# Performance work log

Measured on AMD Instinct MI355X. Metric: run time of the kernel, lower is better.

## Reference

```python
import jax, jax.numpy as jnp
import numpy as np

B, T, NMELS = 2, 2048, 64
D, H, DH, M, L = 256, 4, 64, 384, 4
FF2 = 2 * 4 * D  # GLU doubles the 4*dim hidden


def _layernorm(x, g, b):
    m = x.mean(-1, keepdims=True)
    v = ((x - m) ** 2).mean(-1, keepdims=True)
    return (x - m) * jax.lax.rsqrt(v + 1e-5) * g + b


def _conv(h, w, groups=1, pad='VALID'):
    return jax.lax.conv_general_dilated(h, w, (1, 1), pad, feature_group_count=groups,
                                        dimension_numbers=('NCHW', 'OIHW', 'NCHW'))


def _bn(h, g, b, m, v):
    return (h - m[:, None, None]) * jax.lax.rsqrt(v[:, None, None] + 1e-5) * g[:, None, None] + b[:, None, None]


def setup_inputs():
    key = jax.random.key(0)
    ks = jax.random.split(key, 40)
    def n(i, shape, s):
        return (jax.random.normal(ks[i], shape) * s).astype(jnp.float32)
    z = lambda shape: jnp.zeros(shape, jnp.float32)
    o = lambda shape: jnp.ones(shape, jnp.float32)
    return dict(
        x=n(0, (B, T, NMELS), 1.0),
        conv0_w=n(1, (4, 1, 1, 1), 0.5),
        dw1_w=n(2, (4, 1, 3, 3), 0.3), dw1_b=z(4),
        pw1_w=n(3, (D // 2, 4, 1, 1), 0.5), pw1_b=z(D // 2),
        bn1_g=o(D // 2), bn1_b=z(D // 2), bn1_m=n(4, (D // 2,), 0.05), bn1_v=o(D // 2),
        dw2_w=n(5, (D // 2, 1, 3, 3), 0.3), dw2_b=z(D // 2),
        pw2_w=n(6, (D, D // 2, 1, 1), 0.1), pw2_b=z(D),
        bn2_g=o(D), bn2_b=z(D), bn2_m=n(7, (D,), 0.05), bn2_v=o(D),
        proj_w=n(8, (D, D), 0.06), proj_b=z(D),
        ln0_g=o(D), ln0_b=z(D),
        pos_emb=n(9, (1, T, D), 0.02),
        ln1_g=o((L, D)), ln1_b=z((L, D)),
        wq=n(10, (L, D, D), 0.06), bq=z((L, D)),
        wk=n(11, (L, D, D), 0.06), bk=z((L, D)),
        wv=n(12, (L, D, D), 0.06), bv=z((L, D)),
        wo=n(13, (L, D, D), 0.06), bo=z((L, D)),
        proj_mat=n(14, (L, M, DH), 1.0),
        ln2_g=o((L, D)), ln2_b=z((L, D)),
        ffw1=n(15, (L, D, FF2), 0.06), ffb1=z((L, FF2)),
        ffw2=n(16, (L, FF2 // 2, D), 0.03), ffb2=z((L, D)),
        clf_w1=n(17, (D, D // 2), 0.06), clf_b1=z(D // 2),
        clf_ln_g=o(D // 2), clf_ln_b=z(D // 2),
        clf_w2=n(18, (D // 2, 1), 0.09), clf_b2=z(1),
    )


def reference(x, conv0_w, dw1_w, dw1_b, pw1_w, pw1_b, bn1_g, bn1_b, bn1_m, bn1_v,
              dw2_w, dw2_b, pw2_w, pw2_b, bn2_g, bn2_b, bn2_m, bn2_v,
              proj_w, proj_b, ln0_g, ln0_b, pos_emb,
              ln1_g, ln1_b, wq, bq, wk, bk, wv, bv, wo, bo, proj_mat,
              ln2_g, ln2_b, ffw1, ffb1, ffw2, ffb2,
              clf_w1, clf_b1, clf_ln_g, clf_ln_b, clf_w2, clf_b2):
    pad1 = ((1, 1), (1, 1))
    # conv frontend: [B,T,n_mels] -> [B,1,n_mels,T]
    h = x.transpose(0, 2, 1)[:, None]
    h = _conv(h, conv0_w)
    h = _conv(h, dw1_w, groups=4, pad=pad1) + dw1_b[:, None, None]
    h = _conv(h, pw1_w) + pw1_b[:, None, None]
    h = jax.nn.relu(_bn(h, bn1_g, bn1_b, bn1_m, bn1_v))
    h = _conv(h, dw2_w, groups=D // 2, pad=pad1) + dw2_b[:, None, None]
    h = _conv(h, pw2_w) + pw2_b[:, None, None]
    h = jax.nn.relu(_bn(h, bn2_g, bn2_b, bn2_m, bn2_v))
    h = h.mean(axis=2).transpose(0, 2, 1)  # [B,T,D]
    h = h @ proj_w + proj_b
    h = _layernorm(h, ln0_g, ln0_b) + pos_emb[:, :h.shape[1]]
    # reversible Performer: streams x1 (attn) / x2 (ff), combined by sum
    x1, x2 = h, h
    dn = DH ** -0.25
    for l in range(L):
        a = _layernorm(x2, ln1_g[l], ln1_b[l])
        Bsz, N, _ = a.shape
        q = (a @ wq[l] + bq[l]).reshape(Bsz, N, H, DH).transpose(0, 2, 1, 3)
        k = (a @ wk[l] + bk[l]).reshape(Bsz, N, H, DH).transpose(0, 2, 1, 3)
        v = (a @ wv[l] + bv[l]).reshape(Bsz, N, H, DH).transpose(0, 2, 1, 3)
        # FAVOR+ generalized (ReLU) kernel feature maps, eps=1e-3
        qf = jax.nn.relu(jnp.einsum('bhnd,jd->bhnj', dn * q, proj_mat[l])) + 1e-3
        kf = jax.nn.relu(jnp.einsum('bhnd,jd->bhnj', dn * k, proj_mat[l])) + 1e-3
        d_inv = 1.0 / jnp.einsum('bhnj,bhj->bhn', qf, kf.sum(axis=2))
        ctx = jnp.einsum('bhnj,bhnd->bhjd', kf, v)
        o = jnp.einsum('bhjd,bhnj,bhn->bhnd', ctx, qf, d_inv)
        o = o.transpose(0, 2, 1, 3).reshape(Bsz, N, D)
        x1 = x1 + (o @ wo[l] + bo[l])
        f = _layernorm(x1, ln2_g[l], ln2_b[l])
        u1, u2 = jnp.split(f @ ffw1[l] + ffb1[l], 2, axis=-1)
        x2 = x2 + (jax.nn.gelu(u1, approximate=False) * u2) @ ffw2[l] + ffb2[l]
    h = x1 + x2
    c = jax.nn.relu(_layernorm(h @ clf_w1 + clf_b1, clf_ln_g, clf_ln_b))
    return (c @ clf_w2 + clf_b2)[..., 0]
```

## Files before the change

kernel.cpp:

```cpp
#include <hip/hip_runtime.h>
#include <hip/hip_bf16.h>
#include <math.h>

using bf16 = __hip_bfloat16;
typedef __attribute__((ext_vector_type(8))) short short8;
typedef __attribute__((ext_vector_type(4))) float f32x4;

__device__ __forceinline__ float tof(float x) { return x; }
__device__ __forceinline__ float tof(bf16 x) { return __bfloat162float(x); }
__device__ __forceinline__ float b2f(unsigned short u) {
  union { float f; unsigned int i; } c; c.i = ((unsigned int)u) << 16; return c.f;
}
__device__ __forceinline__ unsigned short f2bu(float v) {
  bf16 h = __float2bfloat16(v);
  return *(unsigned short*)&h;
}
__device__ __forceinline__ void sto1(float* p, float v) { *p = v; }
__device__ __forceinline__ void sto1(bf16* p, float v) { *p = __float2bfloat16(v); }

__device__ __forceinline__ float gelu_exact(float x) {
  return 0.5f * x * (1.f + erff(x * 0.70710678118654752f));
}

__device__ __forceinline__ void llds16(const bf16* g, short* l) {
  __builtin_amdgcn_global_load_lds((const __attribute__((address_space(1))) void*)g,
                                   (__attribute__((address_space(3))) void*)l, 16, 0, 0);
}


__global__ __launch_bounds__(256) void pack_qkv3_kernel(
    const float* __restrict__ wq, const float* __restrict__ wk,
    const float* __restrict__ wv, bf16* __restrict__ out)
{
  int idx = blockIdx.x * 256 + threadIdx.x;
  int k = idx & 255;
  int nl = idx >> 8;
  int n = nl % 768, l = nl / 768;
  const float* src = (n < 256) ? wq : (n < 512 ? wk : wv);
  float v = src[(long)l * 65536 + k * 256 + (n & 255)];
  unsigned short hi = f2bu(v);
  unsigned short lo = f2bu(v - b2f(hi));
  unsigned short* o = (unsigned short*)out + (long)l * 589824 + (long)n * 768;
  o[k] = hi; o[256 + k] = hi; o[512 + k] = lo;
}

__global__ __launch_bounds__(256) void pack_qkvbias_kernel(
    const float* __restrict__ bq, const float* __restrict__ bk,
    const float* __restrict__ bv, float* __restrict__ out)
{
  int i = blockIdx.x * 256 + threadIdx.x;
  if (i >= 3072) return;
  int n = i % 768, l = i / 768;
  const float* src = (n < 256) ? bq : (n < 512 ? bk : bv);
  out[i] = src[l * 256 + (n & 255)];
}

__global__ __launch_bounds__(256) void tconv_kernel(
    const float* __restrict__ in, bf16* __restrict__ out,
    int K, int N, long sin, long sout)
{
  int l = blockIdx.z;
  int idx = blockIdx.x * 256 + threadIdx.x;
  int k = idx % K, n = idx / K;
  out[l * sout + idx] = __float2bfloat16(in[l * sin + (long)k * N + n]);
}

__global__ __launch_bounds__(256) void tconv3_kernel(
    const float* __restrict__ in, bf16* __restrict__ out,
    int K, int N, long sin, long sout)
{
  int l = blockIdx.z;
  int idx = blockIdx.x * 256 + threadIdx.x;
  int k = idx % K, n = idx / K;
  float v = in[l * sin + (long)k * N + n];
  unsigned short hi = f2bu(v);
  unsigned short lo = f2bu(v - b2f(hi));
  unsigned short* o = (unsigned short*)out + l * sout + (long)n * (3 * K);
  o[k] = hi; o[K + k] = hi; o[2 * K + k] = lo;
}

__global__ __launch_bounds__(256) void f2b_kernel(
    const float* __restrict__ in, bf16* __restrict__ out, int n)
{
  int i = blockIdx.x * 256 + threadIdx.x;
  if (i < n) out[i] = __float2bfloat16(in[i]);
}

__global__ __launch_bounds__(256) void zero4_kernel(float* __restrict__ p) {
  int i = (blockIdx.x * 256 + threadIdx.x) * 4;
  float4 z; z.x = 0.f; z.y = 0.f; z.z = 0.f; z.w = 0.f;
  *(float4*)&p[i] = z;
}

__global__ __launch_bounds__(256) void sumb3_kernel(
    const float* __restrict__ a, const float* __restrict__ b, bf16* __restrict__ o)
{
  int row = blockIdx.x, c = threadIdx.x;
  long i = (long)row * 256 + c;
  float v = a[i] + b[i];
  unsigned short hi = f2bu(v);
  unsigned short lo = f2bu(v - b2f(hi));
  unsigned short* op = (unsigned short*)o + (long)row * 768 + c;
  op[0] = hi; op[256] = lo; op[512] = hi;
}

__global__ __launch_bounds__(256) void front1_kernel(
    const float* __restrict__ x, const float* __restrict__ c0w,
    const float* __restrict__ d1w, const float* __restrict__ d1b,
    const float* __restrict__ p1w, const float* __restrict__ p1b,
    const float* __restrict__ g1, const float* __restrict__ b1,
    const float* __restrict__ m1, const float* __restrict__ v1,
    bf16* __restrict__ A1)
{
  __shared__ float sd[256];
  __shared__ float ss[128], st[128], sb[128];
  int tid = threadIdx.x;
  int bt = ((blockIdx.x & 7) << 9) | (blockIdx.x >> 3);
  int b = bt >> 11, t = bt & 2047;
  if (tid < 128) {
    float s = g1[tid] * rsqrtf(v1[tid] + 1e-5f);
    ss[tid] = s;
    st[tid] = b1[tid] - m1[tid] * s;
    sb[tid] = p1b[tid];
  }
  {
    int c = tid >> 6, f = tid & 63;
    float cw = c0w[c];
    float acc = d1b[c];
#pragma unroll
    for (int kh = 0; kh < 3; ++kh) {
      int fi = f + kh - 1;
      if (fi < 0 || fi >= 64) continue;
#pragma unroll
      for (int kw = 0; kw < 3; ++kw) {
        int ti = t + kw - 1;
        if (ti < 0 || ti >= 2048) continue;
        acc += d1w[c * 9 + kh * 3 + kw] * cw * x[((long)b * 2048 + ti) * 64 + fi];
      }
    }
    sd[c * 64 + f] = acc;
  }
  int ci0 = (tid * 8) & 127;
  float wreg[8][4];
#pragma unroll
  for (int j = 0; j < 8; ++j) {
    f32x4 w4 = *(const f32x4*)&p1w[(ci0 + j) * 4];
#pragma unroll
    for (int c = 0; c < 4; ++c) wreg[j][c] = w4[c];
  }
  __syncthreads();
  float ssr[8], str[8], sbr[8];
#pragma unroll
  for (int j = 0; j < 8; ++j) {
    ssr[j] = ss[ci0 + j]; str[j] = st[ci0 + j]; sbr[j] = sb[ci0 + j];
  }
  long ob = (long)bt * 8192;
  unsigned short* A1u = (unsigned short*)A1;
#pragma unroll
  for (int it = 0; it < 4; ++it) {
    int f = it * 16 + (tid >> 4);
    float sdv[4];
#pragma unroll
    for (int c = 0; c < 4; ++c) sdv[c] = sd[c * 64 + f];
    short8 pkt;
#pragma unroll
    for (int j = 0; j < 8; ++j) {
      float pre = sbr[j];
#pragma unroll
      for (int c = 0; c < 4; ++c) pre = fmaf(wreg[j][c], sdv[c], pre);
      pkt[j] = (short)f2bu(fmaxf(fmaf(ssr[j], pre, str[j]), 0.f));
    }
    *(short8*)&A1u[ob + it * 2048 + tid * 8] = pkt;
  }
}

__global__ __launch_bounds__(256, 4) void convtail_kernel(
    const bf16* __restrict__ A1, const float* __restrict__ w,
    const float* __restrict__ wb, const bf16* __restrict__ w2b,
    const float* __restrict__ pb, const float* __restrict__ g2,
    const float* __restrict__ b2, const float* __restrict__ m2,
    const float* __restrict__ v2, bf16* __restrict__ hconv3)
{
  __shared__ short dw2s[64 * 136];
  __shared__ short Bs[64 * 136];
  __shared__ float red[1024];
  __shared__ float ssc[64], ssh[64];
  int tid = threadIdx.x;
  int lane = tid & 63, wv = tid >> 6;
  int quad = lane >> 4, l15 = lane & 15;
  int rw = (wv >> 1) * 32, cw = (wv & 1) * 32;
  int bt = ((blockIdx.x & 7) << 9) | (blockIdx.x >> 3);
  int b = bt >> 11, t = bt & 2047;
  int ci8 = (tid & 15) * 8;
  float wreg[9][8], breg[8];
#pragma unroll
  for (int c = 0; c < 8; ++c) {
    breg[c] = wb[ci8 + c];
#pragma unroll
    for (int kk = 0; kk < 9; ++kk) wreg[kk][c] = w[(ci8 + c) * 9 + kk];
  }
  const unsigned short* A1u = (const unsigned short*)A1;
  for (int pass = 0; pass < 4; ++pass) {
    int f = pass * 16 + (tid >> 4);
    float a[8];
#pragma unroll
    for (int c = 0; c < 8; ++c) a[c] = breg[c];
#pragma unroll
    for (int kh = 0; kh < 3; ++kh) {
      int fi = f + kh - 1;
      if (fi < 0 || fi >= 64) continue;
#pragma unroll
      for (int kw = 0; kw < 3; ++kw) {
        int ti = t + kw - 1;
        if (ti < 0 || ti >= 2048) continue;
        short8 u = *(const short8*)&A1u[(((long)b * 2048 + ti) * 64 + fi) * 128 + ci8];
        int kk = kh * 3 + kw;
#pragma unroll
        for (int c = 0; c < 8; ++c)
          a[c] = fmaf(wreg[kk][c], b2f((unsigned short)u[c]), a[c]);
      }
    }
    short8 p;
#pragma unroll
    for (int c = 0; c < 8; ++c) p[c] = (short)f2bu(a[c]);
    *(short8*)&dw2s[f * 136 + ci8] = p;
  }
  for (int ct = 0; ct < 4; ++ct) {
    int co0 = ct * 64;
    __syncthreads();
    for (int l2 = 0; l2 < 4; ++l2) {
      int idx = l2 * 256 + tid;
      int row = idx >> 4, koff = (idx & 15) * 8;
      *(short8*)&Bs[row * 136 + koff] =
          *(const short8*)&w2b[(long)(co0 + row) * 128 + koff];
    }
    if (tid < 64) {
      int co = co0 + tid;
      float s = g2[co] * rsqrtf(v2[co] + 1e-5f);
      ssc[tid] = s;
      ssh[tid] = b2[co] - m2[co] * s + s * pb[co];
    }
    __syncthreads();
    f32x4 zv = {0.f, 0.f, 0.f, 0.f};
    f32x4 acc[2][2] = {{zv, zv}, {zv, zv}};
#pragma unroll
    for (int kc = 0; kc < 4; ++kc) {
      short8 a0 = *(const short8*)&dw2s[(rw + l15) * 136 + kc * 32 + quad * 8];
      short8 a1 = *(const short8*)&dw2s[(rw + 16 + l15) * 136 + kc * 32 + quad * 8];
      short8 b0 = *(const short8*)&Bs[(cw + l15) * 136 + kc * 32 + quad * 8];
      short8 b1 = *(const short8*)&Bs[(cw + 16 + l15) * 136 + kc * 32 + quad * 8];
      acc[0][0] = __builtin_amdgcn_mfma_f32_16x16x32_bf16(a0, b0, acc[0][0], 0, 0, 0);
      acc[0][1] = __builtin_amdgcn_mfma_f32_16x16x32_bf16(a0, b1, acc[0][1], 0, 0, 0);
      acc[1][0] = __builtin_amdgcn_mfma_f32_16x16x32_bf16(a1, b0, acc[1][0], 0, 0, 0);
      acc[1][1] = __builtin_amdgcn_mfma_f32_16x16x32_bf16(a1, b1, acc[1][1], 0, 0, 0);
    }
#pragma unroll
    for (int mi = 0; mi < 2; ++mi)
#pragma unroll
      for (int nj = 0; nj < 2; ++nj) {
        int colg = cw + nj * 16 + l15;
        float s = ssc[colg], sh = ssh[colg];
        float sum = 0.f;
#pragma unroll
        for (int r = 0; r < 4; ++r) sum += fmaxf(fmaf(s, acc[mi][nj][r], sh), 0.f);
        int rowgroup = (wv >> 1) * 8 + mi * 4 + quad;
        red[rowgroup * 64 + colg] = sum;
      }
    __syncthreads();
    if (tid < 64) {
      float s = 0.f;
#pragma unroll
      for (int r = 0; r < 16; ++r) s += red[r * 64 + tid];
      float vo = s * (1.f / 64.f);
      unsigned short hi = f2bu(vo);
      unsigned short lo = f2bu(vo - b2f(hi));
      unsigned short* hp = (unsigned short*)hconv3 + (long)bt * 768 + co0 + tid;
      hp[0] = hi; hp[256] = lo; hp[512] = hi;
    }
  }
}

__global__ __launch_bounds__(256) void favor_kernel(
    const bf16* __restrict__ qkvb, const bf16* __restrict__ pm,
    bf16* __restrict__ qf, bf16* __restrict__ kfT, float dn)
{
  __shared__ short As[4096];
  __shared__ short Bs[4096];
  int tid = threadIdx.x;
  int lane = tid & 63, w = tid >> 6;
  int quad = lane >> 4, l15 = lane & 15;
  int rw = (w >> 1) * 32, cw = (w & 1) * 32;
  int r0 = blockIdx.x * 64, n0 = blockIdx.y * 64;
  int z16 = blockIdx.z;
  bool isK = z16 >= 8;
  int z = z16 & 7, zb = z >> 2, zh = z & 3;
  const bf16* A = qkvb + (isK ? 256 : 0) + (long)zb * 1048576 + zh * 64;
  f32x4 zv = {0.f, 0.f, 0.f, 0.f};
  f32x4 acc[2][2] = {{zv, zv}, {zv, zv}};
  const bf16* Ag = A + (long)(r0 + (tid >> 2)) * 512 + ((tid & 3) * 8);
  const bf16* Bg = pm + (long)(n0 + (tid >> 2)) * 64 + ((tid & 3) * 8);
  llds16(Ag, &As[tid * 8]);
  llds16(Ag + 32, &As[tid * 8 + 2048]);
  llds16(Bg, &Bs[tid * 8]);
  llds16(Bg + 32, &Bs[tid * 8 + 2048]);
  __syncthreads();
#pragma unroll
  for (int c = 0; c < 2; ++c) {
    short8 a0 = *(const short8*)&As[c * 2048 + (rw + l15) * 32 + quad * 8];
    short8 a1 = *(const short8*)&As[c * 2048 + (rw + 16 + l15) * 32 + quad * 8];
    short8 b0 = *(const short8*)&Bs[c * 2048 + (cw + l15) * 32 + quad * 8];
    short8 b1 = *(const short8*)&Bs[c * 2048 + (cw + 16 + l15) * 32 + quad * 8];
    acc[0][0] = __builtin_amdgcn_mfma_f32_16x16x32_bf16(a0, b0, acc[0][0], 0, 0, 0);
    acc[0][1] = __builtin_amdgcn_mfma_f32_16x16x32_bf16(a0, b1, acc[0][1], 0, 0, 0);
    acc[1][0] = __builtin_amdgcn_mfma_f32_16x16x32_bf16(a1, b0, acc[1][0], 0, 0, 0);
    acc[1][1] = __builtin_amdgcn_mfma_f32_16x16x32_bf16(a1, b1, acc[1][1], 0, 0, 0);
  }
  bf16* qfz = qf + (long)zb * 3145728 + (long)zh * 786432;
  unsigned short* kfz = (unsigned short*)kfT + (long)zb * 3145728 + (long)zh * 786432;
#pragma unroll
  for (int mi = 0; mi < 2; ++mi)
#pragma unroll
    for (int nj = 0; nj < 2; ++nj) {
      int colg = n0 + cw + nj * 16 + l15;
      int rbase = r0 + rw + mi * 16 + quad * 4;
      float ov[4];
#pragma unroll
      for (int r = 0; r < 4; ++r)
        ov[r] = fmaxf(acc[mi][nj][r] * dn, 0.f) + 1e-3f;
      if (!isK) {
#pragma unroll
        for (int r = 0; r < 4; ++r)
          qfz[(long)(rbase + r) * 384 + colg] = __float2bfloat16(ov[r]);
      } else {
        ushort4 p;
        p.x = f2bu(ov[0]); p.y = f2bu(ov[1]); p.z = f2bu(ov[2]); p.w = f2bu(ov[3]);
        *(ushort4*)&kfz[(long)colg * 2048 + rbase] = p;
      }
    }
}

__global__ __launch_bounds__(256) void rowsum_kernel(
    const bf16* __restrict__ kfT, float* __restrict__ ksum)
{
  int z = blockIdx.x;
  int j = blockIdx.y * 4 + (threadIdx.x >> 6);
  int lane = threadIdx.x & 63;
  const short* base = (const short*)kfT + ((long)z * 384 + j) * 2048;
  float acc = 0.f;
#pragma unroll
  for (int i = 0; i < 4; ++i) {
    short8 v = *(const short8*)&base[i * 512 + lane * 8];
#pragma unroll
    for (int e = 0; e < 8; ++e) acc += b2f((unsigned short)v[e]);
  }
#pragma unroll
  for (int o = 32; o > 0; o >>= 1) acc += __shfl_xor(acc, o, 64);
  if (lane == 0) ksum[z * 384 + j] = acc;
}

template <typename CTy, int EPI>
__global__ __launch_bounds__(256) void mgemm_kernel(
    const bf16* __restrict__ A, const bf16* __restrict__ Bt,
    const float* __restrict__ bias, const float* __restrict__ res,
    const float* __restrict__ rowsc, CTy* __restrict__ C, bf16* __restrict__ C2,
    int K, int lda, int ldbt, int ldc,
    long sAb, long sAh, long sBb, long sBh, long sCb, long sCh,
    long sRb, long sRh, int Hdiv, float alpha)
{
  __shared__ short As[4096];
  __shared__ short Bs[4096];
  __shared__ short Bs2[(EPI == 8) ? 4096 : 8];
  int tid = threadIdx.x;
  int lane = tid & 63, w = tid >> 6;
  int quad = lane >> 4, l15 = lane & 15;
  int rw = (w >> 1) * 32, cw = (w & 1) * 32;
  int r0 = blockIdx.x * 64, n0 = blockIdx.y * 64;
  int zb = blockIdx.z / Hdiv, zh = blockIdx.z % Hdiv;
  A += zb * sAb + zh * sAh;
  Bt += zb * sBb + zh * sBh;
  C += zb * sCb + zh * sCh;
  if (res) res += zb * sCb + zh * sCh;
  const float* rsp = (EPI == 3) ? rowsc + zb * sRb + zh * sRh : nullptr;
  f32x4 zv = {0.f, 0.f, 0.f, 0.f};
  f32x4 acc[2][2] = {{zv, zv}, {zv, zv}};
  f32x4 acc2[2][2] = {{zv, zv}, {zv, zv}};
  const bf16* Ag = A + (long)(r0 + (tid >> 2)) * lda + ((tid & 3) * 8);
  const bf16* Bg = Bt + (long)(n0 + (tid >> 2)) * ldbt + ((tid & 3) * 8);
  const bf16* Bg2 = (EPI == 8) ? Bg + sRb : nullptr;
  short* Asd = &As[tid * 8];
  short* Bsd = &Bs[tid * 8];
  short* Bs2d = &Bs2[(EPI == 8) ? tid * 8 : 0];
  for (int k0 = 0; k0 < K; k0 += 64) {
    if (k0) __syncthreads();
    llds16(Ag + k0, Asd);
    llds16(Ag + k0 + 32, Asd + 2048);
    llds16(Bg + k0, Bsd);
    llds16(Bg + k0 + 32, Bsd + 2048);
    if constexpr (EPI == 8) {
      llds16(Bg2 + k0, Bs2d);
      llds16(Bg2 + k0 + 32, Bs2d + 2048);
    }
    __syncthreads();
#pragma unroll
    for (int c = 0; c < 2; ++c) {
      short8 a0 = *(const short8*)&As[c * 2048 + (rw + l15) * 32 + quad * 8];
      short8 a1 = *(const short8*)&As[c * 2048 + (rw + 16 + l15) * 32 + quad * 8];
      short8 b0 = *(const short8*)&Bs[c * 2048 + (cw + l15) * 32 + quad * 8];
      short8 b1 = *(const short8*)&Bs[c * 2048 + (cw + 16 + l15) * 32 + quad * 8];
      acc[0][0] = __builtin_amdgcn_mfma_f32_16x16x32_bf16(a0, b0, acc[0][0], 0, 0, 0);
      acc[0][1] = __builtin_amdgcn_mfma_f32_16x16x32_bf16(a0, b1, acc[0][1], 0, 0, 0);
      acc[1][0] = __builtin_amdgcn_mfma_f32_16x16x32_bf16(a1, b0, acc[1][0], 0, 0, 0);
      acc[1][1] = __builtin_amdgcn_mfma_f32_16x16x32_bf16(a1, b1, acc[1][1], 0, 0, 0);
      if constexpr (EPI == 8) {
        short8 c0 = *(const short8*)&Bs2[c * 2048 + (cw + l15) * 32 + quad * 8];
        short8 c1 = *(const short8*)&Bs2[c * 2048 + (cw + 16 + l15) * 32 + quad * 8];
        acc2[0][0] = __builtin_amdgcn_mfma_f32_16x16x32_bf16(a0, c0, acc2[0][0], 0, 0, 0);
        acc2[0][1] = __builtin_amdgcn_mfma_f32_16x16x32_bf16(a0, c1, acc2[0][1], 0, 0, 0);
        acc2[1][0] = __builtin_amdgcn_mfma_f32_16x16x32_bf16(a1, c0, acc2[1][0], 0, 0, 0);
        acc2[1][1] = __builtin_amdgcn_mfma_f32_16x16x32_bf16(a1, c1, acc2[1][1], 0, 0, 0);
      }
    }
  }
#pragma unroll
  for (int mi = 0; mi < 2; ++mi)
#pragma unroll
    for (int nj = 0; nj < 2; ++nj) {
      int colg = n0 + cw + nj * 16 + l15;
      float bv_ = bias ? bias[colg] : 0.f;
      float bv2 = (EPI == 8) ? bias[colg + 1024] : 0.f;
      int rbase = r0 + rw + mi * 16 + quad * 4;
      float ov[4];
#pragma unroll
      for (int r = 0; r < 4; ++r) {
        float v = acc[mi][nj][r];
        if constexpr (EPI == 0 || EPI == 5) {
          v += bv_;
        } else if constexpr (EPI == 1) {
          v += bv_ + res[(long)(rbase + r) * ldc + colg];
        } else if constexpr (EPI == 3) {
          v *= rsp[rbase + r];
        } else if constexpr (EPI == 7) {
          if (zh == 0) v += bv_;
        } else if constexpr (EPI == 8) {
          v = gelu_exact(v + bv_) * (acc2[mi][nj][r] + bv2);
        }
        ov[r] = v;
      }
      if constexpr (EPI == 5) {
        if (colg < 512) {
#pragma unroll
          for (int r = 0; r < 4; ++r) sto1(&C[(long)(rbase + r) * ldc + colg], ov[r]);
        } else {
          int bb = rbase >> 11, t0 = rbase & 2047;
          long off = (((long)bb * 4 + ((colg - 512) >> 6)) * 64 + (colg & 63)) * 2048 + t0;
          ushort4 p;
          p.x = f2bu(ov[0]); p.y = f2bu(ov[1]); p.z = f2bu(ov[2]); p.w = f2bu(ov[3]);
          *(ushort4*)((unsigned short*)C2 + off) = p;
        }
      } else if constexpr (EPI == 7) {
#pragma unroll
        for (int r = 0; r < 4; ++r)
          atomicAdd((float*)&C[(long)(rbase + r) * ldc + colg], ov[r]);
      } else if constexpr (EPI == 8) {
        unsigned short* Cu = (unsigned short*)C;
#pragma unroll
        for (int r = 0; r < 4; ++r) {
          float v = ov[r];
          unsigned short hi = f2bu(v);
          unsigned short lo = f2bu(v - b2f(hi));
          long rowo = (long)(rbase + r) * ldc;
          Cu[rowo + colg] = hi;
          Cu[rowo + 1024 + colg] = lo;
          Cu[rowo + 2048 + colg] = hi;
        }
      } else {
#pragma unroll
        for (int r = 0; r < 4; ++r) sto1(&C[(long)(rbase + r) * ldc + colg], ov[r]);
      }
    }
  (void)alpha;
}

template <int DIM, bool RELU, bool ADDPOS, bool DUAL, bool A3, typename OTy>
__global__ __launch_bounds__(256) void ln_kernel(
    const float* __restrict__ in, const float* __restrict__ g,
    const float* __restrict__ b, const float* __restrict__ pos,
    OTy* __restrict__ out0, float* __restrict__ out1)
{
  constexpr int CH = DIM / 64;
  int row = blockIdx.x * 4 + (threadIdx.x >> 6);
  int lane = threadIdx.x & 63;
  const float* rp = in + (long)row * DIM + lane * CH;
  float v[CH];
#pragma unroll
  for (int i = 0; i < CH; ++i) v[i] = rp[i];
  float s = 0.f;
#pragma unroll
  for (int i = 0; i < CH; ++i) s += v[i];
#pragma unroll
  for (int o = 32; o > 0; o >>= 1) s += __shfl_xor(s, o, 64);
  float mean = s * (1.f / DIM);
  float q = 0.f;
#pragma unroll
  for (int i = 0; i < CH; ++i) { float d = v[i] - mean; q += d * d; }
#pragma unroll
  for (int o = 32; o > 0; o >>= 1) q += __shfl_xor(q, o, 64);
  float rstd = rsqrtf(q * (1.f / DIM) + 1e-5f);
  int t = row & 2047;
#pragma unroll
  for (int i = 0; i < CH; ++i) {
    int c = lane * CH + i;
    float o = (v[i] - mean) * rstd * g[c] + b[c];
    if constexpr (ADDPOS) o += pos[(long)t * DIM + c];
    if constexpr (RELU) o = fmaxf(o, 0.f);
    if constexpr (A3) {
      unsigned short hi = f2bu(o);
      unsigned short lo = f2bu(o - b2f(hi));
      unsigned short* op = (unsigned short*)out0 + (long)row * (3 * DIM) + c;
      op[0] = hi; op[DIM] = lo; op[2 * DIM] = hi;
    } else {
      sto1(&out0[(long)row * DIM + c], o);
      if constexpr (DUAL) out1[(long)row * DIM + c] = o;
    }
  }
}

__global__ __launch_bounds__(256) void dinv_kernel(
    const bf16* __restrict__ qf, const float* __restrict__ ksum,
    float* __restrict__ dinv)
{
  int z = blockIdx.x;
  int t = blockIdx.y * 4 + (threadIdx.x >> 6);
  int lane = threadIdx.x & 63;
  const bf16* qr = qf + ((long)z * 2048 + t) * 384;
  const float* ks = ksum + z * 384;
  float acc = 0.f;
#pragma unroll
  for (int i = 0; i < 6; ++i) {
    int j = lane + i * 64;
    acc = fmaf(tof(qr[j]), ks[j], acc);
  }
#pragma unroll
  for (int o = 32; o > 0; o >>= 1) acc += __shfl_xor(acc, o, 64);
  if (lane == 0) dinv[z * 2048 + t] = 1.f / acc;
}

__global__ __launch_bounds__(256) void clf2_kernel(
    const float* __restrict__ c2, const float* __restrict__ w,
    const float* __restrict__ b, float* __restrict__ out)
{
  int row = blockIdx.x * 4 + (threadIdx.x >> 6);
  int lane = threadIdx.x & 63;
  const float* rp = c2 + (long)row * 128 + lane * 2;
  float acc = rp[0] * w[lane * 2] + rp[1] * w[lane * 2 + 1];
#pragma unroll
  for (int o = 32; o > 0; o >>= 1) acc += __shfl_xor(acc, o, 64);
  if (lane == 0) out[row] = acc + b[0];
}

extern "C" void kernel_launch(void* const* d_in, const int* in_sizes, int n_in,
                              void* d_out, int out_size, void* d_ws, size_t ws_size,
                              hipStream_t stream)
{
  const float* X    = (const float*)d_in[0];
  const float* c0w  = (const float*)d_in[1];
  const float* d1w  = (const float*)d_in[2];
  const float* d1b  = (const float*)d_in[3];
  const float* p1w  = (const float*)d_in[4];
  const float* p1b  = (const float*)d_in[5];
  const float* g1   = (const float*)d_in[6];
  const float* b1   = (const float*)d_in[7];
  const float* m1   = (const float*)d_in[8];
  const float* v1   = (const float*)d_in[9];
  const float* d2w  = (const float*)d_in[10];
  const float* d2b  = (const float*)d_in[11];
  const float* p2w  = (const float*)d_in[12];
  const float* p2b  = (const float*)d_in[13];
  const float* g2   = (const float*)d_in[14];
  const float* b2   = (const float*)d_in[15];
  const float* m2   = (const float*)d_in[16];
  const float* v2   = (const float*)d_in[17];
  const float* projw= (const float*)d_in[18];
  const float* projb= (const float*)d_in[19];
  const float* ln0g = (const float*)d_in[20];
  const float* ln0b = (const float*)d_in[21];
  const float* pos  = (const float*)d_in[22];
  const float* ln1g = (const float*)d_in[23];
  const float* ln1b = (const float*)d_in[24];
  const float* wq   = (const float*)d_in[25];
  const float* bq   = (const float*)d_in[26];
  const float* wk   = (const float*)d_in[27];
  const float* bk   = (const float*)d_in[28];
  const float* wv   = (const float*)d_in[29];
  const float* bv   = (const float*)d_in[30];
  const float* wo   = (const float*)d_in[31];
  const float* bo   = (const float*)d_in[32];
  const float* pmat = (const float*)d_in[33];
  const float* ln2g = (const float*)d_in[34];
  const float* ln2b = (const float*)d_in[35];
  const float* ffw1 = (const float*)d_in[36];
  const float* ffb1 = (const float*)d_in[37];
  const float* ffw2 = (const float*)d_in[38];
  const float* ffb2 = (const float*)d_in[39];
  const float* cw1  = (const float*)d_in[40];
  const float* cb1  = (const float*)d_in[41];
  const float* clng = (const float*)d_in[42];
  const float* clnb = (const float*)d_in[43];
  const float* cw2  = (const float*)d_in[44];
  const float* cb2  = (const float*)d_in[45];
  (void)in_sizes; (void)n_in; (void)out_size; (void)ws_size;

  float* ws     = (float*)d_ws;
  float* x1     = ws;
  float* x2     = ws + 1048576;
  bf16*  lnA3   = (bf16*)(ws + 2097152);
  bf16*  hconv3 = (bf16*)(ws + 3670016);
  bf16*  A1     = (bf16*)(ws + 5242880);
  bf16*  wqkv3  = (bf16*)(ws + 5242880);
  float* qkvbias= ws + 6422528;
  bf16*  f1w3   = (bf16*)(ws + 6425600);
  bf16*  f2w3   = (bf16*)(ws + 9571328);
  bf16*  wo_bf  = (bf16*)(ws + 11144192);
  bf16*  pm_bf  = (bf16*)(ws + 11275264);
  bf16*  projwT3= (bf16*)(ws + 11324416);
  bf16*  cw1T3  = (bf16*)(ws + 11422720);
  bf16*  qkvb   = (bf16*)(ws + 11471872);
  bf16*  vT     = (bf16*)(ws + 12520448);
  bf16*  qf     = (bf16*)(ws + 13044736);
  bf16*  kfT    = (bf16*)(ws + 16190464);
  bf16*  obufb  = (bf16*)(ws + 19336192);
  float* ctx32  = ws + 19860480;
  float* ksum   = ws + 20057088;
  float* dinvp  = ws + 20061184;
  bf16*  ctxb   = (bf16*)(ws + 20077568);
  float* lnb32  = ws + 20126720;
  float* c1     = ws + 21175296;
  float* c2     = ws + 21699584;
  bf16*  gb2    = qkvb;
  bf16*  sbuf3  = qkvb;
  bf16*  pw2_bf = (bf16*)x1;

  const float dn = 0.35355339059327378f;

  f2b_kernel<<<128, 256, 0, stream>>>(p2w, pw2_bf, 32768);
  front1_kernel<<<4096, 256, 0, stream>>>(X, c0w, d1w, d1b, p1w, p1b, g1, b1, m1, v1, A1);
  convtail_kernel<<<4096, 256, 0, stream>>>(A1, d2w, d2b, pw2_bf, p2b, g2, b2, m2, v2, hconv3);

  pack_qkv3_kernel<<<3072, 256, 0, stream>>>(wq, wk, wv, wqkv3);
  pack_qkvbias_kernel<<<12, 256, 0, stream>>>(bq, bk, bv, qkvbias);
  tconv3_kernel<<<dim3(2048, 1, 4), 256, 0, stream>>>(ffw1, f1w3, 256, 2048, 524288, 1572864);
  tconv3_kernel<<<dim3(1024, 1, 4), 256, 0, stream>>>(ffw2, f2w3, 1024, 256, 262144, 786432);
  tconv_kernel<<<dim3(256, 1, 4), 256, 0, stream>>>(wo, wo_bf, 256, 256, 65536, 65536);
  tconv3_kernel<<<dim3(256, 1, 1), 256, 0, stream>>>(projw, projwT3, 256, 256, 65536, 196608);
  tconv3_kernel<<<dim3(128, 1, 1), 256, 0, stream>>>(cw1, cw1T3, 256, 128, 32768, 98304);
  f2b_kernel<<<384, 256, 0, stream>>>(pmat, pm_bf, 98304);

  mgemm_kernel<float, 0><<<dim3(64, 4, 1), 256, 0, stream>>>(
      hconv3, projwT3, projb, nullptr, nullptr, lnb32, nullptr,
      768, 768, 768, 256, 0, 0, 0, 0, 0, 0, 0, 0, 1, 1.f);
  ln_kernel<256, false, true, true, false, float><<<1024, 256, 0, stream>>>(
      lnb32, ln0g, ln0b, pos, x1, x2);

  for (int l = 0; l < 4; ++l) {
    const bf16* wqkv_l = wqkv3 + (size_t)l * 589824;
    const float* qb_l  = qkvbias + l * 768;
    const bf16* pm_l   = pm_bf + (size_t)l * 24576;
    const bf16* wo_l   = wo_bf + (size_t)l * 65536;
    const float* bov   = bo + l * 256;
    const bf16* f1w_l  = f1w3 + (size_t)l * 1572864;
    const float* f1b_l = ffb1 + l * 2048;
    const bf16* f2w_l  = f2w3 + (size_t)l * 786432;
    const float* f2b_l = ffb2 + l * 256;

    ln_kernel<256, false, false, false, true, bf16><<<1024, 256, 0, stream>>>(
        x2, ln1g + l * 256, ln1b + l * 256, nullptr, lnA3, nullptr);
    mgemm_kernel<bf16, 5><<<dim3(64, 12, 1), 256, 0, stream>>>(
        lnA3, wqkv_l, qb_l, nullptr, nullptr, qkvb, vT,
        768, 768, 768, 512, 0, 0, 0, 0, 0, 0, 0, 0, 1, 1.f);
    zero4_kernel<<<192, 256, 0, stream>>>(ctx32);
    favor_kernel<<<dim3(32, 6, 16), 256, 0, stream>>>(
        qkvb, pm_l, qf, kfT, dn);
    rowsum_kernel<<<dim3(8, 96), 256, 0, stream>>>(kfT, ksum);
    dinv_kernel<<<dim3(8, 512), 256, 0, stream>>>(qf, ksum, dinvp);
    mgemm_kernel<float, 7><<<dim3(1, 6, 64), 256, 0, stream>>>(
        vT, kfT, nullptr, nullptr, nullptr, ctx32, nullptr,
        256, 2048, 2048, 384, 131072, 256, 786432, 256, 24576, 0, 0, 0, 8, 1.f);
    f2b_kernel<<<768, 256, 0, stream>>>(ctx32, ctxb, 196608);
    mgemm_kernel<bf16, 3><<<dim3(32, 1, 8), 256, 0, stream>>>(
        qf, ctxb, nullptr, nullptr, dinvp, obufb, nullptr,
        384, 384, 384, 256, 3145728, 786432, 98304, 24576, 524288, 64, 8192, 2048, 4, 1.f);
    mgemm_kernel<float, 7><<<dim3(64, 4, 2), 256, 0, stream>>>(
        obufb, wo_l, bov, nullptr, nullptr, x1, nullptr,
        128, 256, 256, 256, 0, 128, 0, 128, 0, 0, 0, 0, 2, 1.f);
    ln_kernel<256, false, false, false, true, bf16><<<1024, 256, 0, stream>>>(
        x1, ln2g + l * 256, ln2b + l * 256, nullptr, lnA3, nullptr);
    mgemm_kernel<bf16, 8><<<dim3(64, 16, 1), 256, 0, stream>>>(
        lnA3, f1w_l, f1b_l, nullptr, nullptr, gb2, nullptr,
        768, 768, 768, 3072, 0, 0, 0, 0, 0, 0, 786432, 0, 1, 1.f);
    mgemm_kernel<float, 7><<<dim3(64, 4, 4), 256, 0, stream>>>(
        gb2, f2w_l, f2b_l, nullptr, nullptr, x2, nullptr,
        768, 3072, 3072, 256, 0, 768, 0, 768, 0, 0, 0, 0, 4, 1.f);
  }

  sumb3_kernel<<<4096, 256, 0, stream>>>(x1, x2, sbuf3);
  mgemm_kernel<float, 0><<<dim3(64, 2, 1), 256, 0, stream>>>(
      sbuf3, cw1T3, cb1, nullptr, nullptr, c1, nullptr,
      768, 768, 768, 128, 0, 0, 0, 0, 0, 0, 0, 0, 1, 1.f);
  ln_kernel<128, true, false, false, false, float><<<1024, 256, 0, stream>>>(
      c1, clng, clnb, nullptr, c2, nullptr);
  clf2_kernel<<<1024, 256, 0, stream>>>(c2, cw2, cb2, (float*)d_out);
}
```

Baseline: 787.5 us.

## Pre-swizzle conv weights for direct MFMA loads, fuse ksum and zeroing into neighbors

A new prep kernel stores the pointwise conv2 weights in MFMA fragment order, so convtail reads B operands straight from global memory. This removes the per-tile LDS staging and one barrier per tile. BN scale and shift for all 256 channels are computed once per block, and the reduction buffer is double-buffered. The key-feature row sums are now accumulated with atomics inside favor_kernel, and the ctx/ksum zeroing is folded into the preceding layernorm launch, which removes two launches per layer. The cost is extra global atomics and uncoalesced fragment reads from global memory inside convtail.

```diff
diff --git a/kernel.cpp b/kernel.cpp
--- a/kernel.cpp
+++ b/kernel.cpp
@@ -86,10 +86,19 @@
   if (i < n) out[i] = __float2bfloat16(in[i]);
 }
 
-__global__ __launch_bounds__(256) void zero4_kernel(float* __restrict__ p) {
-  int i = (blockIdx.x * 256 + threadIdx.x) * 4;
-  float4 z; z.x = 0.f; z.y = 0.f; z.z = 0.f; z.w = 0.f;
-  *(float4*)&p[i] = z;
+__global__ __launch_bounds__(256) void bprep2_kernel(
+    const float* __restrict__ p2w, bf16* __restrict__ out)
+{
+  int idx = blockIdx.x * 256 + threadIdx.x;
+  int j = idx & 7;
+  int lane = (idx >> 3) & 63;
+  int nj = (idx >> 9) & 1;
+  int cww = (idx >> 10) & 1;
+  int kc = (idx >> 11) & 3;
+  int ct = (idx >> 13) & 3;
+  int co = ct * 64 + cww * 32 + nj * 16 + (lane & 15);
+  int k = kc * 32 + (lane >> 4) * 8 + j;
+  out[idx] = __float2bfloat16(p2w[co * 128 + k]);
 }
 
 __global__ __launch_bounds__(256) void sumb3_kernel(
@@ -176,15 +185,14 @@
 
 __global__ __launch_bounds__(256, 4) void convtail_kernel(
     const bf16* __restrict__ A1, const float* __restrict__ w,
-    const float* __restrict__ wb, const bf16* __restrict__ w2b,
+    const float* __restrict__ wb, const bf16* __restrict__ Bq,
     const float* __restrict__ pb, const float* __restrict__ g2,
     const float* __restrict__ b2, const float* __restrict__ m2,
     const float* __restrict__ v2, bf16* __restrict__ hconv3)
 {
   __shared__ short dw2s[64 * 136];
-  __shared__ short Bs[64 * 136];
-  __shared__ float red[1024];
-  __shared__ float ssc[64], ssh[64];
+  __shared__ float ssc[256], ssh[256];
+  __shared__ float red[2][16][65];
   int tid = threadIdx.x;
   int lane = tid & 63, wv = tid >> 6;
   int quad = lane >> 4, l15 = lane & 15;
@@ -199,6 +207,11 @@
 #pragma unroll
     for (int kk = 0; kk < 9; ++kk) wreg[kk][c] = w[(ci8 + c) * 9 + kk];
   }
+  {
+    float s = g2[tid] * rsqrtf(v2[tid] + 1e-5f);
+    ssc[tid] = s;
+    ssh[tid] = b2[tid] - m2[tid] * s + s * pb[tid];
+  }
   const unsigned short* A1u = (const unsigned short*)A1;
   for (int pass = 0; pass < 4; ++pass) {
     int f = pass * 16 + (tid >> 4);
@@ -225,56 +238,45 @@
     for (int c = 0; c < 8; ++c) p[c] = (short)f2bu(a[c]);
     *(short8*)&dw2s[f * 136 + ci8] = p;
   }
+  __syncthreads();
+  const unsigned short* Bqu = (const unsigned short*)Bq;
   for (int ct = 0; ct < 4; ++ct) {
-    int co0 = ct * 64;
-    __syncthreads();
-    for (int l2 = 0; l2 < 4; ++l2) {
-      int idx = l2 * 256 + tid;
-      int row = idx >> 4, koff = (idx & 15) * 8;
-      *(short8*)&Bs[row * 136 + koff] =
-          *(const short8*)&w2b[(long)(co0 + row) * 128 + koff];
-    }
-    if (tid < 64) {
-      int co = co0 + tid;
-      float s = g2[co] * rsqrtf(v2[co] + 1e-5f);
-      ssc[tid] = s;
-      ssh[tid] = b2[co] - m2[co] * s + s * pb[co];
-    }
-    __syncthreads();
     f32x4 zv = {0.f, 0.f, 0.f, 0.f};
     f32x4 acc[2][2] = {{zv, zv}, {zv, zv}};
 #pragma unroll
     for (int kc = 0; kc < 4; ++kc) {
       short8 a0 = *(const short8*)&dw2s[(rw + l15) * 136 + kc * 32 + quad * 8];
       short8 a1 = *(const short8*)&dw2s[(rw + 16 + l15) * 136 + kc * 32 + quad * 8];
-      short8 b0 = *(const short8*)&Bs[(cw + l15) * 136 + kc * 32 + quad * 8];
-      short8 b1 = *(const short8*)&Bs[(cw + 16 + l15) * 136 + kc * 32 + quad * 8];
+      long bb = ((((long)(ct * 4 + kc) * 2 + (cw >> 5)) * 2) * 64 + lane) * 8;
+      short8 b0 = *(const short8*)&Bqu[bb];
+      short8 b1 = *(const short8*)&Bqu[bb + 512];
       acc[0][0] = __builtin_amdgcn_mfma_f32_16x16x32_bf16(a0, b0, acc[0][0], 0, 0, 0);
       acc[0][1] = __builtin_amdgcn_mfma_f32_16x16x32_bf16(a0, b1, acc[0][1], 0, 0, 0);
       acc[1][0] = __builtin_amdgcn_mfma_f32_16x16x32_bf16(a1, b0, acc[1][0], 0, 0, 0);
       acc[1][1] = __builtin_amdgcn_mfma_f32_16x16x32_bf16(a1, b1, acc[1][1], 0, 0, 0);
     }
+    int p = ct & 1;
 #pragma unroll
     for (int mi = 0; mi < 2; ++mi)
 #pragma unroll
       for (int nj = 0; nj < 2; ++nj) {
         int colg = cw + nj * 16 + l15;
-        float s = ssc[colg], sh = ssh[colg];
+        int co = ct * 64 + colg;
+        float s = ssc[co], sh = ssh[co];
         float sum = 0.f;
 #pragma unroll
         for (int r = 0; r < 4; ++r) sum += fmaxf(fmaf(s, acc[mi][nj][r], sh), 0.f);
-        int rowgroup = (wv >> 1) * 8 + mi * 4 + quad;
-        red[rowgroup * 64 + colg] = sum;
+        red[p][(wv >> 1) * 8 + mi * 4 + quad][colg] = sum;
       }
     __syncthreads();
     if (tid < 64) {
       float s = 0.f;
 #pragma unroll
-      for (int r = 0; r < 16; ++r) s += red[r * 64 + tid];
+      for (int r = 0; r < 16; ++r) s += red[p][r][tid];
       float vo = s * (1.f / 64.f);
       unsigned short hi = f2bu(vo);
       unsigned short lo = f2bu(vo - b2f(hi));
-      unsigned short* hp = (unsigned short*)hconv3 + (long)bt * 768 + co0 + tid;
+      unsigned short* hp = (unsigned short*)hconv3 + (long)bt * 768 + ct * 64 + tid;
       hp[0] = hi; hp[256] = lo; hp[512] = hi;
     }
   }
@@ -282,7 +284,8 @@
 
 __global__ __launch_bounds__(256) void favor_kernel(
     const bf16* __restrict__ qkvb, const bf16* __restrict__ pm,
-    bf16* __restrict__ qf, bf16* __restrict__ kfT, float dn)
+    bf16* __restrict__ qf, bf16* __restrict__ kfT, float* __restrict__ ksum,
+    float dn)
 {
   __shared__ short As[4096];
   __shared__ short Bs[4096];
@@ -335,27 +338,12 @@
         ushort4 p;
         p.x = f2bu(ov[0]); p.y = f2bu(ov[1]); p.z = f2bu(ov[2]); p.w = f2bu(ov[3]);
         *(ushort4*)&kfz[(long)colg * 2048 + rbase] = p;
+        float s = b2f(p.x) + b2f(p.y) + b2f(p.z) + b2f(p.w);
+        s += __shfl_xor(s, 16, 64);
+        s += __shfl_xor(s, 32, 64);
+        if (quad == 0) atomicAdd(&ksum[z * 384 + colg], s);
       }
     }
-}
-
-__global__ __launch_bounds__(256) void rowsum_kernel(
-    const bf16* __restrict__ kfT, float* __restrict__ ksum)
-{
-  int z = blockIdx.x;
-  int j = blockIdx.y * 4 + (threadIdx.x >> 6);
-  int lane = threadIdx.x & 63;
-  const short* base = (const short*)kfT + ((long)z * 384 + j) * 2048;
-  float acc = 0.f;
-#pragma unroll
-  for (int i = 0; i < 4; ++i) {
-    short8 v = *(const short8*)&base[i * 512 + lane * 8];
-#pragma unroll
-    for (int e = 0; e < 8; ++e) acc += b2f((unsigned short)v[e]);
-  }
-#pragma unroll
-  for (int o = 32; o > 0; o >>= 1) acc += __shfl_xor(acc, o, 64);
-  if (lane == 0) ksum[z * 384 + j] = acc;
 }
 
 template <typename CTy, int EPI>
@@ -435,8 +423,6 @@
         float v = acc[mi][nj][r];
         if constexpr (EPI == 0 || EPI == 5) {
           v += bv_;
-        } else if constexpr (EPI == 1) {
-          v += bv_ + res[(long)(rbase + r) * ldc + colg];
         } else if constexpr (EPI == 3) {
           v *= rsp[rbase + r];
         } else if constexpr (EPI == 7) {
@@ -485,8 +471,16 @@
 __global__ __launch_bounds__(256) void ln_kernel(
     const float* __restrict__ in, const float* __restrict__ g,
     const float* __restrict__ b, const float* __restrict__ pos,
-    OTy* __restrict__ out0, float* __restrict__ out1)
-{
+    OTy* __restrict__ out0, float* __restrict__ out1,
+    float4* __restrict__ zaux, int zn4)
+{
+  if (zaux) {
+    int gid = blockIdx.x * 256 + threadIdx.x;
+    if (gid < zn4) {
+      float4 z; z.x = 0.f; z.y = 0.f; z.z = 0.f; z.w = 0.f;
+      zaux[gid] = z;
+    }
+  }
   constexpr int CH = DIM / 64;
   int row = blockIdx.x * 4 + (threadIdx.x >> 6);
   int lane = threadIdx.x & 63;
@@ -638,13 +632,13 @@
   float* c2     = ws + 21699584;
   bf16*  gb2    = qkvb;
   bf16*  sbuf3  = qkvb;
-  bf16*  pw2_bf = (bf16*)x1;
+  bf16*  Bq     = (bf16*)x1;
 
   const float dn = 0.35355339059327378f;
 
-  f2b_kernel<<<128, 256, 0, stream>>>(p2w, pw2_bf, 32768);
+  bprep2_kernel<<<128, 256, 0, stream>>>(p2w, Bq);
   front1_kernel<<<4096, 256, 0, stream>>>(X, c0w, d1w, d1b, p1w, p1b, g1, b1, m1, v1, A1);
-  convtail_kernel<<<4096, 256, 0, stream>>>(A1, d2w, d2b, pw2_bf, p2b, g2, b2, m2, v2, hconv3);
+  convtail_kernel<<<4096, 256, 0, stream>>>(A1, d2w, d2b, Bq, p2b, g2, b2, m2, v2, hconv3);
 
   pack_qkv3_kernel<<<3072, 256, 0, stream>>>(wq, wk, wv, wqkv3);
   pack_qkvbias_kernel<<<12, 256, 0, stream>>>(bq, bk, bv, qkvbias);
@@ -659,7 +653,7 @@
       hconv3, projwT3, projb, nullptr, nullptr, lnb32, nullptr,
       768, 768, 768, 256, 0, 0, 0, 0, 0, 0, 0, 0, 1, 1.f);
   ln_kernel<256, false, true, true, false, float><<<1024, 256, 0, stream>>>(
-      lnb32, ln0g, ln0b, pos, x1, x2);
+      lnb32, ln0g, ln0b, pos, x1, x2, nullptr, 0);
 
   for (int l = 0; l < 4; ++l) {
     const bf16* wqkv_l = wqkv3 + (size_t)l * 589824;
@@ -673,14 +667,13 @@
     const float* f2b_l = ffb2 + l * 256;
 
     ln_kernel<256, false, false, false, true, bf16><<<1024, 256, 0, stream>>>(
-        x2, ln1g + l * 256, ln1b + l * 256, nullptr, lnA3, nullptr);
+        x2, ln1g + l * 256, ln1b + l * 256, nullptr, lnA3, nullptr,
+        (float4*)ctx32, 50176);
     mgemm_kernel<bf16, 5><<<dim3(64, 12, 1), 256, 0, stream>>>(
         lnA3, wqkv_l, qb_l, nullptr, nullptr, qkvb, vT,
         768, 768, 768, 512, 0, 0, 0, 0, 0, 0, 0, 0, 1, 1.f);
-    zero4_kernel<<<192, 256, 0, stream>>>(ctx32);
     favor_kernel<<<dim3(32, 6, 16), 256, 0, stream>>>(
-        qkvb, pm_l, qf, kfT, dn);
-    rowsum_kernel<<<dim3(8, 96), 256, 0, stream>>>(kfT, ksum);
+        qkvb, pm_l, qf, kfT, ksum, dn);
     dinv_kernel<<<dim3(8, 512), 256, 0, stream>>>(qf, ksum, dinvp);
     mgemm_kernel<float, 7><<<dim3(1, 6, 64), 256, 0, stream>>>(
         vT, kfT, nullptr, nullptr, nullptr, ctx32, nullptr,
@@ -693,7 +686,7 @@
         obufb, wo_l, bov, nullptr, nullptr, x1, nullptr,
         128, 256, 256, 256, 0, 128, 0, 128, 0, 0, 0, 0, 2, 1.f);
     ln_kernel<256, false, false, false, true, bf16><<<1024, 256, 0, stream>>>(
-        x1, ln2g + l * 256, ln2b + l * 256, nullptr, lnA3, nullptr);
+        x1, ln2g + l * 256, ln2b + l * 256, nullptr, lnA3, nullptr, nullptr, 0);
     mgemm_kernel<bf16, 8><<<dim3(64, 16, 1), 256, 0, stream>>>(
         lnA3, f1w_l, f1b_l, nullptr, nullptr, gb2, nullptr,
         768, 768, 768, 3072, 0, 0, 0, 0, 0, 0, 786432, 0, 1, 1.f);
@@ -707,6 +700,6 @@
       sbuf3, cw1T3, cb1, nullptr, nullptr, c1, nullptr,
       768, 768, 768, 128, 0, 0, 0, 0, 0, 0, 0, 0, 1, 1.f);
   ln_kernel<128, true, false, false, false, float><<<1024, 256, 0, stream>>>(
-      c1, clng, clnb, nullptr, c2, nullptr);
+      c1, clng, clnb, nullptr, c2, nullptr, nullptr, 0);
   clf2_kernel<<<1024, 256, 0, stream>>>(c2, cw2, cb2, (float*)d_out);
 }
```

New measurement: 794.5 us. Within noise of the previous version (+0.9%).
